# Kernel tuning notes

Measured on AMD Instinct MI355X. Metric: run time of the kernel, lower is better.

Reference implementation:

```python
import jax, jax.numpy as jnp
import numpy as np

B, S, I, H, O = 64, 512, 256, 1024, 256


def setup_inputs() -> dict:
    key = jax.random.key(0)
    ks = jax.random.split(key, 12)
    s_in = 1.0 / np.sqrt(H)  # torch RNN init scale
    inp = {
        "x": jax.random.normal(ks[0], (B, S, I), dtype=jnp.float32),
        "W_ih_0": jax.random.uniform(ks[1], (H, I), jnp.float32, -s_in, s_in),
        "W_hh_0": jax.random.uniform(ks[2], (H, H), jnp.float32, -s_in, s_in),
        "b_ih_0": jax.random.uniform(ks[3], (H,), jnp.float32, -s_in, s_in),
        "b_hh_0": jax.random.uniform(ks[4], (H,), jnp.float32, -s_in, s_in),
        "W_ih_1": jax.random.uniform(ks[5], (H, H), jnp.float32, -s_in, s_in),
        "W_hh_1": jax.random.uniform(ks[6], (H, H), jnp.float32, -s_in, s_in),
        "b_ih_1": jax.random.uniform(ks[7], (H,), jnp.float32, -s_in, s_in),
        "b_hh_1": jax.random.uniform(ks[8], (H,), jnp.float32, -s_in, s_in),
        "fc_w": jax.random.uniform(ks[9], (O, H), jnp.float32, -s_in, s_in),
        "fc_b": jax.random.uniform(ks[10], (O,), jnp.float32, -s_in, s_in),
    }
    return inp


def _rnn_layer(inp, W_ih, W_hh, b_ih, b_hh):
    # Pre-compute input projection for all timesteps (one big GEMM),
    # then scan the sequential recurrence: h_t = tanh(Wx_t + U h_{t-1} + b)
    pre = jnp.einsum('bsi,hi->bsh', inp, W_ih) + (b_ih + b_hh)  # [B,S,H]
    h0 = jnp.zeros((inp.shape[0], W_hh.shape[0]), dtype=inp.dtype)

    def step(h, p_t):
        h = jnp.tanh(p_t + h @ W_hh.T)
        return h, h

    _, hs = jax.lax.scan(step, h0, jnp.swapaxes(pre, 0, 1))  # [S,B,H]
    return jnp.swapaxes(hs, 0, 1)  # [B,S,H]


def reference(x, W_ih_0, W_hh_0, b_ih_0, b_hh_0,
              W_ih_1, W_hh_1, b_ih_1, b_hh_1, fc_w, fc_b):
    h = _rnn_layer(x, W_ih_0, W_hh_0, b_ih_0, b_hh_0)
    h = _rnn_layer(h, W_ih_1, W_hh_1, b_ih_1, b_hh_1)
    return h @ fc_w.T + fc_b  # [B,S,O]
```

## Files before the change

### kernel.cpp

```cpp
#include <hip/hip_runtime.h>
#include <hip/hip_bf16.h>


typedef __attribute__((ext_vector_type(4))) float f32x4;
typedef __attribute__((ext_vector_type(8))) short bf16x8;
typedef __attribute__((ext_vector_type(4))) int   i32x4;
typedef __attribute__((ext_vector_type(4))) short s16x4;

#define B_  64
#define S_  512
#define I_  256
#define H_  1024
#define O_  256
#define M_  (B_ * S_)
#define SH_ (S_ * H_)

static __device__ __forceinline__ unsigned short f2bf(float f) {
  union { float f; unsigned u; } v; v.f = f;
  unsigned r = v.u + 0x7fffu + ((v.u >> 16) & 1u);
  return (unsigned short)(r >> 16);
}
static __device__ __forceinline__ float bf2f(unsigned short b) {
  union { unsigned u; float f; } v; v.u = ((unsigned)b) << 16;
  return v.f;
}
static __device__ __forceinline__ float tanh_fast(float x) {
  float e = __expf(2.f * x);
  return 1.f - 2.f / (e + 1.f);
}
static __device__ __forceinline__ bf16x8 as_bf16x8(i32x4 v) {
  union { i32x4 i; bf16x8 b; } u; u.i = v; return u.b;
}

__global__ void cvt_bf16(const float* __restrict__ src,
                         unsigned short* __restrict__ dst, int n4) {
  int i = blockIdx.x * blockDim.x + threadIdx.x;
  if (i < n4) {
    f32x4 v = ((const f32x4*)src)[i];
    s16x4 o;
    o[0] = (short)f2bf(v[0]); o[1] = (short)f2bf(v[1]);
    o[2] = (short)f2bf(v[2]); o[3] = (short)f2bf(v[3]);
    ((s16x4*)dst)[i] = o;
  }
}

template <bool BF16OUT>
__global__ __launch_bounds__(256)
void gemm_bf16(const unsigned short* __restrict__ A,
               const unsigned short* __restrict__ W,
               const float* __restrict__ b1, const float* __restrict__ b2,
               void* __restrict__ Cv, int Mx, int Nx, int Kx) {
  __shared__ __align__(16) unsigned short As[128 * 40];
  __shared__ __align__(16) unsigned short Bs[128 * 40];
  const int tid  = threadIdx.x;
  const int m0   = blockIdx.y * 128;
  const int n0   = blockIdx.x * 128;
  const int w    = tid >> 6, lane = tid & 63;
  const int quad = lane >> 4, l15 = lane & 15;
  const int wm = (w & 1) * 64, wn = (w >> 1) * 64;

  f32x4 acc[4][4] = {};

  for (int k0 = 0; k0 < Kx; k0 += 32) {
#pragma unroll
    for (int i = 0; i < 2; ++i) {
      int c = tid + i * 256;
      int row = c >> 2, kc = c & 3;
      *(i32x4*)&As[row * 40 + kc * 8] =
          *(const i32x4*)&A[(size_t)(m0 + row) * Kx + k0 + kc * 8];
      *(i32x4*)&Bs[row * 40 + kc * 8] =
          *(const i32x4*)&W[(size_t)(n0 + row) * Kx + k0 + kc * 8];
    }
    __syncthreads();
    bf16x8 af[4], bg[4];
#pragma unroll
    for (int im = 0; im < 4; ++im)
      af[im] = *(const bf16x8*)&As[(wm + im * 16 + l15) * 40 + quad * 8];
#pragma unroll
    for (int in = 0; in < 4; ++in)
      bg[in] = *(const bf16x8*)&Bs[(wn + in * 16 + l15) * 40 + quad * 8];
#pragma unroll
    for (int im = 0; im < 4; ++im)
#pragma unroll
      for (int in = 0; in < 4; ++in)
        acc[im][in] = __builtin_amdgcn_mfma_f32_16x16x32_bf16(
            af[im], bg[in], acc[im][in], 0, 0, 0);
    __syncthreads();
  }

#pragma unroll
  for (int in = 0; in < 4; ++in) {
    int n = n0 + wn + in * 16 + l15;
    float bv = b1 ? b1[n] : 0.f;
    if (b2) bv += b2[n];
#pragma unroll
    for (int im = 0; im < 4; ++im) {
      int mb = m0 + wm + im * 16 + quad * 4;
#pragma unroll
      for (int r = 0; r < 4; ++r) {
        float val = acc[im][in][r] + bv;
        size_t o = (size_t)(mb + r) * Nx + n;
        if (BF16OUT) ((unsigned short*)Cv)[o] = f2bf(val);
        else         ((float*)Cv)[o] = val;
      }
    }
  }
}

__global__ __launch_bounds__(256, 1)
void rnn_fused(const unsigned short* __restrict__ Whh0,
               const unsigned short* __restrict__ Wih1,
               const unsigned short* __restrict__ Whh1,
               const unsigned short* __restrict__ pre0,
               const float* __restrict__ b_ih_1,
               const float* __restrict__ b_hh_1,
               unsigned short* __restrict__ h0seq,
               unsigned short* __restrict__ h1seq,
               unsigned int* __restrict__ flags)
{
  const int bx   = blockIdx.x;
  const int tid  = threadIdx.x;
  const int w    = tid >> 6;
  const int lane = tid & 63;
  const int quad = lane >> 4, l15 = lane & 15;

  __shared__ __align__(16) float q[4][4][16][20];

  if (bx < 64) {
    const int g  = bx >> 4;
    const int n0 = (bx & 15) * 64;
    unsigned int* const f0 = flags + g * S_;

    i32x4 Wf[4][8];
    {
      const unsigned short* wp = Whh0 + (size_t)(n0 + l15) * H_ + w * 256 + quad * 8;
#pragma unroll
      for (int i = 0; i < 4; ++i)
#pragma unroll
        for (int kk = 0; kk < 8; ++kk)
          Wf[i][kk] = *(const i32x4*)(wp + (size_t)i * 16 * H_ + kk * 32);
    }
#pragma unroll
    for (int i = 0; i < 4; ++i)
#pragma unroll
      for (int kk = 0; kk < 8; ++kk)
        asm volatile("" : "+v"(Wf[i][kk]));

    for (int t = 0; t < S_; ++t) {
      float pv[4];
      {
        const unsigned short* pp = pre0 + (size_t)(g * 16 + quad * 4) * SH_ +
                                   (size_t)t * H_ + n0 + w * 16 + l15;
#pragma unroll
        for (int r = 0; r < 4; ++r) pv[r] = bf2f(pp[(size_t)r * SH_]);
      }

      f32x4 acc[4] = {};
      if (t > 0) {
        if (tid == 0) {
          while (__hip_atomic_load(&f0[t - 1], __ATOMIC_RELAXED,
                                   __HIP_MEMORY_SCOPE_AGENT) < 16u) {}
          __builtin_amdgcn_fence(__ATOMIC_ACQUIRE, "agent");
        }
        __syncthreads();
        const unsigned short* hp = h0seq + (size_t)(g * 16 + l15) * SH_ +
                                   (size_t)(t - 1) * H_ + w * 256 + quad * 8;
        bf16x8 Af[8];
#pragma unroll
        for (int kk = 0; kk < 8; ++kk) Af[kk] = *(const bf16x8*)(hp + kk * 32);
#pragma unroll
        for (int kk = 0; kk < 8; ++kk)
#pragma unroll
          for (int i = 0; i < 4; ++i)
            acc[i] = __builtin_amdgcn_mfma_f32_16x16x32_bf16(
                Af[kk], as_bf16x8(Wf[i][kk]), acc[i], 0, 0, 0);
      }

#pragma unroll
      for (int i = 0; i < 4; ++i) *(f32x4*)&q[w][i][l15][quad * 4] = acc[i];
      __syncthreads();
      f32x4 s = {};
#pragma unroll
      for (int wp2 = 0; wp2 < 4; ++wp2) {
        f32x4 v = *(const f32x4*)&q[wp2][w][l15][quad * 4];
#pragma unroll
        for (int r = 0; r < 4; ++r) s[r] += v[r];
      }

#pragma unroll
      for (int r = 0; r < 4; ++r) {
        unsigned short hb = f2bf(tanh_fast(pv[r] + s[r]));
        size_t o = (size_t)(g * 16 + quad * 4 + r) * SH_ + (size_t)t * H_ +
                   n0 + w * 16 + l15;
        __hip_atomic_store(&h0seq[o], hb, __ATOMIC_RELAXED,
                           __HIP_MEMORY_SCOPE_AGENT);
      }
      __syncthreads();
      if (tid == 0)
        __hip_atomic_fetch_add(&f0[t], 1u, __ATOMIC_RELAXED,
                               __HIP_MEMORY_SCOPE_AGENT);
    }
  } else {
    const int id = bx - 64;
    const int g  = id >> 5;
    const int n0 = (id & 31) * 32;
    unsigned int* const f0 = flags + g * S_;
    unsigned int* const f1 = flags + 4 * S_ + g * S_;

    i32x4 Wi[2][8], Wr[2][8];
    {
      const unsigned short* wpi = Wih1 + (size_t)(n0 + l15) * H_ + w * 256 + quad * 8;
      const unsigned short* wpr = Whh1 + (size_t)(n0 + l15) * H_ + w * 256 + quad * 8;
#pragma unroll
      for (int i = 0; i < 2; ++i)
#pragma unroll
        for (int kk = 0; kk < 8; ++kk) {
          Wi[i][kk] = *(const i32x4*)(wpi + (size_t)i * 16 * H_ + kk * 32);
          Wr[i][kk] = *(const i32x4*)(wpr + (size_t)i * 16 * H_ + kk * 32);
        }
    }
#pragma unroll
    for (int i = 0; i < 2; ++i)
#pragma unroll
      for (int kk = 0; kk < 8; ++kk) {
        asm volatile("" : "+v"(Wi[i][kk]));
        asm volatile("" : "+v"(Wr[i][kk]));
      }

    float bias = 0.f;
    if (w < 2) {
      int n = n0 + w * 16 + l15;
      bias = b_ih_1[n] + b_hh_1[n];
    }

    for (int t = 0; t < S_; ++t) {
      f32x4 acc[2] = {};

      if (tid == 0) {
        while (__hip_atomic_load(&f0[t], __ATOMIC_RELAXED,
                                 __HIP_MEMORY_SCOPE_AGENT) < 16u) {}
        __builtin_amdgcn_fence(__ATOMIC_ACQUIRE, "agent");
      }
      __syncthreads();
      {
        const unsigned short* hp = h0seq + (size_t)(g * 16 + l15) * SH_ +
                                   (size_t)t * H_ + w * 256 + quad * 8;
        bf16x8 Af[8];
#pragma unroll
        for (int kk = 0; kk < 8; ++kk) Af[kk] = *(const bf16x8*)(hp + kk * 32);
#pragma unroll
        for (int kk = 0; kk < 8; ++kk)
#pragma unroll
          for (int i = 0; i < 2; ++i)
            acc[i] = __builtin_amdgcn_mfma_f32_16x16x32_bf16(
                Af[kk], as_bf16x8(Wi[i][kk]), acc[i], 0, 0, 0);
      }

      if (t > 0) {
        if (tid == 0) {
          while (__hip_atomic_load(&f1[t - 1], __ATOMIC_RELAXED,
                                   __HIP_MEMORY_SCOPE_AGENT) < 32u) {}
          __builtin_amdgcn_fence(__ATOMIC_ACQUIRE, "agent");
        }
        __syncthreads();
        const unsigned short* hp = h1seq + (size_t)(g * 16 + l15) * SH_ +
                                   (size_t)(t - 1) * H_ + w * 256 + quad * 8;
        bf16x8 Af[8];
#pragma unroll
        for (int kk = 0; kk < 8; ++kk) Af[kk] = *(const bf16x8*)(hp + kk * 32);
#pragma unroll
        for (int kk = 0; kk < 8; ++kk)
#pragma unroll
          for (int i = 0; i < 2; ++i)
            acc[i] = __builtin_amdgcn_mfma_f32_16x16x32_bf16(
                Af[kk], as_bf16x8(Wr[i][kk]), acc[i], 0, 0, 0);
      }

#pragma unroll
      for (int i = 0; i < 2; ++i) *(f32x4*)&q[w][i][l15][quad * 4] = acc[i];
      __syncthreads();
      if (w < 2) {
        f32x4 s = {};
#pragma unroll
        for (int wp2 = 0; wp2 < 4; ++wp2) {
          f32x4 v = *(const f32x4*)&q[wp2][w][l15][quad * 4];
#pragma unroll
          for (int r = 0; r < 4; ++r) s[r] += v[r];
        }
#pragma unroll
        for (int r = 0; r < 4; ++r) {
          unsigned short hb = f2bf(tanh_fast(bias + s[r]));
          size_t o = (size_t)(g * 16 + quad * 4 + r) * SH_ + (size_t)t * H_ +
                     n0 + w * 16 + l15;
          __hip_atomic_store(&h1seq[o], hb, __ATOMIC_RELAXED,
                             __HIP_MEMORY_SCOPE_AGENT);
        }
      }
      __syncthreads();
      if (tid == 0)
        __hip_atomic_fetch_add(&f1[t], 1u, __ATOMIC_RELAXED,
                               __HIP_MEMORY_SCOPE_AGENT);
    }
  }
}

extern "C" void kernel_launch(void* const* d_in, const int* in_sizes, int n_in,
                              void* d_out, int out_size, void* d_ws, size_t ws_size,
                              hipStream_t stream) {
  const float* x      = (const float*)d_in[0];
  const float* W_ih_0 = (const float*)d_in[1];
  const float* W_hh_0 = (const float*)d_in[2];
  const float* b_ih_0 = (const float*)d_in[3];
  const float* b_hh_0 = (const float*)d_in[4];
  const float* W_ih_1 = (const float*)d_in[5];
  const float* W_hh_1 = (const float*)d_in[6];
  const float* b_ih_1 = (const float*)d_in[7];
  const float* b_hh_1 = (const float*)d_in[8];
  const float* fc_w   = (const float*)d_in[9];
  const float* fc_b   = (const float*)d_in[10];
  float* out = (float*)d_out;

  char* ws = (char*)d_ws;
  size_t off = 0;
  auto alloc = [&](size_t bytes) { char* p = ws + off; off += (bytes + 255) & ~(size_t)255; return p; };
  unsigned short* xb    = (unsigned short*)alloc((size_t)M_ * I_ * 2);
  unsigned short* wih0b = (unsigned short*)alloc((size_t)H_ * I_ * 2);
  unsigned short* whh0b = (unsigned short*)alloc((size_t)H_ * H_ * 2);
  unsigned short* wih1b = (unsigned short*)alloc((size_t)H_ * H_ * 2);
  unsigned short* whh1b = (unsigned short*)alloc((size_t)H_ * H_ * 2);
  unsigned short* fcwb  = (unsigned short*)alloc((size_t)O_ * H_ * 2);
  unsigned int*   flags = (unsigned int*)alloc(2 * 4 * S_ * 4);
  unsigned short* pre0b = (unsigned short*)alloc((size_t)M_ * H_ * 2);
  unsigned short* h0seq = (unsigned short*)alloc((size_t)M_ * H_ * 2);
  unsigned short* h1seq = (unsigned short*)alloc((size_t)M_ * H_ * 2);

  hipMemsetAsync(flags, 0, 2 * 4 * S_ * 4, stream);

  auto cvt = [&](const float* s, unsigned short* d, int n) {
    int n4 = n / 4;
    cvt_bf16<<<(n4 + 255) / 256, 256, 0, stream>>>(s, d, n4);
  };
  cvt(x,      xb,    M_ * I_);
  cvt(W_ih_0, wih0b, H_ * I_);
  cvt(W_hh_0, whh0b, H_ * H_);
  cvt(W_ih_1, wih1b, H_ * H_);
  cvt(W_hh_1, whh1b, H_ * H_);
  cvt(fc_w,   fcwb,  O_ * H_);

  gemm_bf16<true><<<dim3(H_ / 128, M_ / 128), 256, 0, stream>>>(
      xb, wih0b, b_ih_0, b_hh_0, pre0b, M_, H_, I_);

  rnn_fused<<<192, 256, 0, stream>>>(whh0b, wih1b, whh1b, pre0b,
                                     b_ih_1, b_hh_1, h0seq, h1seq, flags);

  gemm_bf16<false><<<dim3(O_ / 128, M_ / 128), 256, 0, stream>>>(
      h1seq, fcwb, fc_b, nullptr, out, M_, O_, H_);
}
```

Baseline: 2.813 ms.

## Pin each RNN batch group to one XCD and use per-block step signals

Launches 256 blocks and keeps only even residues mod 8, so each batch group is meant to land on a single XCD. A startup handshake reads the hardware XCC id to confirm this placement. When placement is confirmed, hidden-state stores become plain stores instead of agent-scope atomics. Per-producer monotonic signal slots with min-polling and s_sleep replace the shared fetch-add counters. Layer-1 blocks now each cover 64 columns instead of 32, using all four waves. This adds a placement check with a timeout fallback. Plain stores rely on the XCD-local L2 being coherent for other blocks on the same XCD, and layer-1 register pressure is higher.

```diff
diff --git a/kernel.cpp b/kernel.cpp
--- a/kernel.cpp
+++ b/kernel.cpp
@@ -14,6 +14,8 @@
 #define O_  256
 #define M_  (B_ * S_)
 #define SH_ (S_ * H_)
+#define NACT 128
+#define POISON_TAG 0xFFu
 
 static __device__ __forceinline__ unsigned short f2bf(float f) {
   union { float f; unsigned u; } v; v.f = f;
@@ -30,6 +32,33 @@
 }
 static __device__ __forceinline__ bf16x8 as_bf16x8(i32x4 v) {
   union { i32x4 i; bf16x8 b; } u; u.i = v; return u.b;
+}
+
+
+static __device__ __forceinline__ void wait16(const unsigned* sig, int v) {
+  for (;;) {
+    unsigned mn = 0xffffffffu;
+#pragma unroll
+    for (int i = 0; i < 16; ++i) {
+      unsigned x = __hip_atomic_load(&sig[i], __ATOMIC_RELAXED,
+                                     __HIP_MEMORY_SCOPE_AGENT);
+      mn = x < mn ? x : mn;
+    }
+    if (mn >= (unsigned)v) break;
+    __builtin_amdgcn_s_sleep(2);
+  }
+  __builtin_amdgcn_fence(__ATOMIC_ACQUIRE, "agent");
+}
+
+static __device__ __forceinline__ void sig_store(unsigned* p, int v) {
+  __hip_atomic_store(p, (unsigned)v, __ATOMIC_RELAXED,
+                     __HIP_MEMORY_SCOPE_AGENT);
+}
+
+static __device__ __forceinline__ void h_store(unsigned short* p,
+                                               unsigned short v, bool local) {
+  if (local) *p = v;
+  else __hip_atomic_store(p, v, __ATOMIC_RELAXED, __HIP_MEMORY_SCOPE_AGENT);
 }
 
 __global__ void cvt_bf16(const float* __restrict__ src,
@@ -118,22 +147,71 @@
                unsigned short* __restrict__ h1seq,
                unsigned int* __restrict__ flags)
 {
-  const int bx   = blockIdx.x;
-  const int tid  = threadIdx.x;
+  const int bx  = blockIdx.x;
+  const int res = bx & 7;
+  if (res & 1) return;
+  const int g   = res >> 1;
+  const int r   = bx >> 3;
+  const int tid = threadIdx.x;
   const int w    = tid >> 6;
   const int lane = tid & 63;
   const int quad = lane >> 4, l15 = lane & 15;
-
+  const int n0   = (r & 15) * 64;
+
+  unsigned* xcdtab = flags;
+  unsigned* sigA = flags + 128 + (g * 3 + 0) * 16;
+  unsigned* sigB = flags + 128 + (g * 3 + 1) * 16;
+  unsigned* sigC = flags + 128 + (g * 3 + 2) * 16;
+
+  __shared__ int s_local;
   __shared__ __align__(16) float q[4][4][16][20];
 
-  if (bx < 64) {
-    const int g  = bx >> 4;
-    const int n0 = (bx & 15) * 64;
-    unsigned int* const f0 = flags + g * S_;
-
+  if (tid == 0) {
+    unsigned tag =
+        ((unsigned)__builtin_amdgcn_s_getreg((3 << 11) | 20) & 0xFu) + 1u;
+    __hip_atomic_store(&xcdtab[g * 32 + r], tag, __ATOMIC_RELEASE,
+                       __HIP_MEMORY_SCOPE_AGENT);
+    unsigned long long t0 = __builtin_amdgcn_s_memrealtime();
+    bool timeout = false;
+    for (;;) {
+      bool all = true;
+      for (int i = 0; i < NACT; ++i)
+        if (__hip_atomic_load(&xcdtab[i], __ATOMIC_RELAXED,
+                              __HIP_MEMORY_SCOPE_AGENT) == 0u) {
+          all = false; break;
+        }
+      if (all) break;
+      if (__builtin_amdgcn_s_memrealtime() - t0 > 5000000ull) {
+        timeout = true; break;
+      }
+      __builtin_amdgcn_s_sleep(8);
+    }
+    int verdict = 0;
+    if (timeout) {
+      __hip_atomic_store(&xcdtab[g * 32 + r], POISON_TAG, __ATOMIC_RELAXED,
+                         __HIP_MEMORY_SCOPE_AGENT);
+    } else {
+      __builtin_amdgcn_fence(__ATOMIC_ACQUIRE, "agent");
+      bool loc = true;
+      int  cnt = 0;
+      for (int i = 0; i < NACT; ++i) {
+        unsigned v = __hip_atomic_load(&xcdtab[i], __ATOMIC_RELAXED,
+                                       __HIP_MEMORY_SCOPE_AGENT);
+        if ((i >> 5) == g) loc &= (v == tag);
+        cnt += (v == tag) ? 1 : 0;
+      }
+      verdict = (loc && cnt == 32) ? 1 : 0;
+    }
+    s_local = verdict;
+  }
+  __syncthreads();
+  const bool local = (s_local != 0);
+
+  if (r < 16) {
     i32x4 Wf[4][8];
     {
-      const unsigned short* wp = Whh0 + (size_t)(n0 + l15) * H_ + w * 256 + quad * 8;
+      const unsigned short* wp =
+          Whh0 + (size_t)(n0 + l15) * H_ + w * 256 + quad * 8;
 #pragma unroll
       for (int i = 0; i < 4; ++i)
 #pragma unroll
@@ -152,16 +230,12 @@
         const unsigned short* pp = pre0 + (size_t)(g * 16 + quad * 4) * SH_ +
                                    (size_t)t * H_ + n0 + w * 16 + l15;
 #pragma unroll
-        for (int r = 0; r < 4; ++r) pv[r] = bf2f(pp[(size_t)r * SH_]);
+        for (int u = 0; u < 4; ++u) pv[u] = bf2f(pp[(size_t)u * SH_]);
       }
 
       f32x4 acc[4] = {};
       if (t > 0) {
-        if (tid == 0) {
-          while (__hip_atomic_load(&f0[t - 1], __ATOMIC_RELAXED,
-                                   __HIP_MEMORY_SCOPE_AGENT) < 16u) {}
-          __builtin_amdgcn_fence(__ATOMIC_ACQUIRE, "agent");
-        }
+        if (tid == 0) wait16(sigA, t);
         __syncthreads();
         const unsigned short* hp = h0seq + (size_t)(g * 16 + l15) * SH_ +
                                    (size_t)(t - 1) * H_ + w * 256 + quad * 8;
@@ -184,35 +258,32 @@
       for (int wp2 = 0; wp2 < 4; ++wp2) {
         f32x4 v = *(const f32x4*)&q[wp2][w][l15][quad * 4];
 #pragma unroll
-        for (int r = 0; r < 4; ++r) s[r] += v[r];
-      }
-
-#pragma unroll
-      for (int r = 0; r < 4; ++r) {
-        unsigned short hb = f2bf(tanh_fast(pv[r] + s[r]));
-        size_t o = (size_t)(g * 16 + quad * 4 + r) * SH_ + (size_t)t * H_ +
+        for (int u = 0; u < 4; ++u) s[u] += v[u];
+      }
+
+#pragma unroll
+      for (int u = 0; u < 4; ++u) {
+        unsigned short hb = f2bf(tanh_fast(pv[u] + s[u]));
+        size_t o = (size_t)(g * 16 + quad * 4 + u) * SH_ + (size_t)t * H_ +
                    n0 + w * 16 + l15;
-        __hip_atomic_store(&h0seq[o], hb, __ATOMIC_RELAXED,
-                           __HIP_MEMORY_SCOPE_AGENT);
+        h_store(&h0seq[o], hb, local);
       }
       __syncthreads();
-      if (tid == 0)
-        __hip_atomic_fetch_add(&f0[t], 1u, __ATOMIC_RELAXED,
-                               __HIP_MEMORY_SCOPE_AGENT);
+      if (tid == 0) {
+        sig_store(&sigA[r], t + 1);
+        sig_store(&sigB[r], t + 1);
+      }
     }
   } else {
-    const int id = bx - 64;
-    const int g  = id >> 5;
-    const int n0 = (id & 31) * 32;
-    unsigned int* const f0 = flags + g * S_;
-    unsigned int* const f1 = flags + 4 * S_ + g * S_;
-
-    i32x4 Wi[2][8], Wr[2][8];
+    const int p1 = r - 16;
+    i32x4 Wi[4][8], Wr[4][8];
     {
-      const unsigned short* wpi = Wih1 + (size_t)(n0 + l15) * H_ + w * 256 + quad * 8;
-      const unsigned short* wpr = Whh1 + (size_t)(n0 + l15) * H_ + w * 256 + quad * 8;
-#pragma unroll
-      for (int i = 0; i < 2; ++i)
+      const unsigned short* wpi =
+          Wih1 + (size_t)(n0 + l15) * H_ + w * 256 + quad * 8;
+      const unsigned short* wpr =
+          Whh1 + (size_t)(n0 + l15) * H_ + w * 256 + quad * 8;
+#pragma unroll
+      for (int i = 0; i < 4; ++i)
 #pragma unroll
         for (int kk = 0; kk < 8; ++kk) {
           Wi[i][kk] = *(const i32x4*)(wpi + (size_t)i * 16 * H_ + kk * 32);
@@ -220,27 +291,23 @@
         }
     }
 #pragma unroll
-    for (int i = 0; i < 2; ++i)
+    for (int i = 0; i < 4; ++i)
 #pragma unroll
       for (int kk = 0; kk < 8; ++kk) {
         asm volatile("" : "+v"(Wi[i][kk]));
         asm volatile("" : "+v"(Wr[i][kk]));
       }
 
-    float bias = 0.f;
-    if (w < 2) {
+    float bias;
+    {
       int n = n0 + w * 16 + l15;
       bias = b_ih_1[n] + b_hh_1[n];
     }
 
     for (int t = 0; t < S_; ++t) {
-      f32x4 acc[2] = {};
-
-      if (tid == 0) {
-        while (__hip_atomic_load(&f0[t], __ATOMIC_RELAXED,
-                                 __HIP_MEMORY_SCOPE_AGENT) < 16u) {}
-        __builtin_amdgcn_fence(__ATOMIC_ACQUIRE, "agent");
-      }
+      f32x4 acc[4] = {};
+
+      if (tid == 0) wait16(sigB, t + 1);
       __syncthreads();
       {
         const unsigned short* hp = h0seq + (size_t)(g * 16 + l15) * SH_ +
@@ -251,17 +318,13 @@
 #pragma unroll
         for (int kk = 0; kk < 8; ++kk)
 #pragma unroll
-          for (int i = 0; i < 2; ++i)
+          for (int i = 0; i < 4; ++i)
             acc[i] = __builtin_amdgcn_mfma_f32_16x16x32_bf16(
                 Af[kk], as_bf16x8(Wi[i][kk]), acc[i], 0, 0, 0);
       }
 
       if (t > 0) {
-        if (tid == 0) {
-          while (__hip_atomic_load(&f1[t - 1], __ATOMIC_RELAXED,
-                                   __HIP_MEMORY_SCOPE_AGENT) < 32u) {}
-          __builtin_amdgcn_fence(__ATOMIC_ACQUIRE, "agent");
-        }
+        if (tid == 0) wait16(sigC, t);
         __syncthreads();
         const unsigned short* hp = h1seq + (size_t)(g * 16 + l15) * SH_ +
                                    (size_t)(t - 1) * H_ + w * 256 + quad * 8;
@@ -271,35 +334,30 @@
 #pragma unroll
         for (int kk = 0; kk < 8; ++kk)
 #pragma unroll
-          for (int i = 0; i < 2; ++i)
+          for (int i = 0; i < 4; ++i)
             acc[i] = __builtin_amdgcn_mfma_f32_16x16x32_bf16(
                 Af[kk], as_bf16x8(Wr[i][kk]), acc[i], 0, 0, 0);
       }
 
 #pragma unroll
-      for (int i = 0; i < 2; ++i) *(f32x4*)&q[w][i][l15][quad * 4] = acc[i];
+      for (int i = 0; i < 4; ++i) *(f32x4*)&q[w][i][l15][quad * 4] = acc[i];
       __syncthreads();
-      if (w < 2) {
-        f32x4 s = {};
-#pragma unroll
-        for (int wp2 = 0; wp2 < 4; ++wp2) {
-          f32x4 v = *(const f32x4*)&q[wp2][w][l15][quad * 4];
-#pragma unroll
-          for (int r = 0; r < 4; ++r) s[r] += v[r];
-        }
-#pragma unroll
-        for (int r = 0; r < 4; ++r) {
-          unsigned short hb = f2bf(tanh_fast(bias + s[r]));
-          size_t o = (size_t)(g * 16 + quad * 4 + r) * SH_ + (size_t)t * H_ +
-                     n0 + w * 16 + l15;
-          __hip_atomic_store(&h1seq[o], hb, __ATOMIC_RELAXED,
-                             __HIP_MEMORY_SCOPE_AGENT);
-        }
+      f32x4 s = {};
+#pragma unroll
+      for (int wp2 = 0; wp2 < 4; ++wp2) {
+        f32x4 v = *(const f32x4*)&q[wp2][w][l15][quad * 4];
+#pragma unroll
+        for (int u = 0; u < 4; ++u) s[u] += v[u];
+      }
+#pragma unroll
+      for (int u = 0; u < 4; ++u) {
+        unsigned short hb = f2bf(tanh_fast(bias + s[u]));
+        size_t o = (size_t)(g * 16 + quad * 4 + u) * SH_ + (size_t)t * H_ +
+                   n0 + w * 16 + l15;
+        h_store(&h1seq[o], hb, local);
       }
       __syncthreads();
-      if (tid == 0)
-        __hip_atomic_fetch_add(&f1[t], 1u, __ATOMIC_RELAXED,
-                               __HIP_MEMORY_SCOPE_AGENT);
+      if (tid == 0) sig_store(&sigC[p1], t + 1);
     }
   }
 }
@@ -329,12 +387,12 @@
   unsigned short* wih1b = (unsigned short*)alloc((size_t)H_ * H_ * 2);
   unsigned short* whh1b = (unsigned short*)alloc((size_t)H_ * H_ * 2);
   unsigned short* fcwb  = (unsigned short*)alloc((size_t)O_ * H_ * 2);
-  unsigned int*   flags = (unsigned int*)alloc(2 * 4 * S_ * 4);
+  unsigned int*   flags = (unsigned int*)alloc(320 * 4);
   unsigned short* pre0b = (unsigned short*)alloc((size_t)M_ * H_ * 2);
   unsigned short* h0seq = (unsigned short*)alloc((size_t)M_ * H_ * 2);
   unsigned short* h1seq = (unsigned short*)alloc((size_t)M_ * H_ * 2);
 
-  hipMemsetAsync(flags, 0, 2 * 4 * S_ * 4, stream);
+  hipMemsetAsync(flags, 0, 320 * 4, stream);
 
   auto cvt = [&](const float* s, unsigned short* d, int n) {
     int n4 = n / 4;
@@ -350,7 +408,7 @@
   gemm_bf16<true><<<dim3(H_ / 128, M_ / 128), 256, 0, stream>>>(
       xb, wih0b, b_ih_0, b_hh_0, pre0b, M_, H_, I_);
 
-  rnn_fused<<<192, 256, 0, stream>>>(whh0b, wih1b, whh1b, pre0b,
+  rnn_fused<<<256, 256, 0, stream>>>(whh0b, wih1b, whh1b, pre0b,
                                      b_ih_1, b_hh_1, h0seq, h1seq, flags);
 
   gemm_bf16<false><<<dim3(O_ / 128, M_ / 128), 256, 0, stream>>>(
```

New measurement: 4.914 ms. 74.7% more time.

## Stage recurrent weights in LDS and load hidden state with cache-bypass loads

Applied to the files above, without the earlier changes.

Moves the per-block recurrent weight slices from pinned VGPRs into a 128KB LDS buffer read on every MFMA. Hidden-state reads now go through inline asm global loads with sc0 sc1 bits, so they are served from a coherent cache level rather than a possibly stale L2. It also adds an explicit vmcnt drain and release ordering on the flag increment so the producer's stores are visible before consumers are signalled. This frees many registers and fixes a cross-block visibility hazard, but adds LDS traffic and waits in the serial per-step critical path.

```diff
diff --git a/kernel.cpp b/kernel.cpp
--- a/kernel.cpp
+++ b/kernel.cpp
@@ -30,6 +30,28 @@
 }
 static __device__ __forceinline__ bf16x8 as_bf16x8(i32x4 v) {
   union { i32x4 i; bf16x8 b; } u; u.i = v; return u.b;
+}
+
+static __device__ __forceinline__ void load8_llc(const unsigned short* p,
+                                                 i32x4* o) {
+  asm volatile(
+      "global_load_dwordx4 %0, %8, off sc0 sc1\n\t"
+      "global_load_dwordx4 %1, %8, off offset:64 sc0 sc1\n\t"
+      "global_load_dwordx4 %2, %8, off offset:128 sc0 sc1\n\t"
+      "global_load_dwordx4 %3, %8, off offset:192 sc0 sc1\n\t"
+      "global_load_dwordx4 %4, %8, off offset:256 sc0 sc1\n\t"
+      "global_load_dwordx4 %5, %8, off offset:320 sc0 sc1\n\t"
+      "global_load_dwordx4 %6, %8, off offset:384 sc0 sc1\n\t"
+      "global_load_dwordx4 %7, %8, off offset:448 sc0 sc1\n\t"
+      "s_waitcnt vmcnt(0)"
+      : "=&v"(o[0]), "=&v"(o[1]), "=&v"(o[2]), "=&v"(o[3]),
+        "=&v"(o[4]), "=&v"(o[5]), "=&v"(o[6]), "=&v"(o[7])
+      : "v"(p)
+      : "memory");
+}
+
+static __device__ __forceinline__ void drain_stores() {
+  asm volatile("s_waitcnt vmcnt(0)" ::: "memory");
 }
 
 __global__ void cvt_bf16(const float* __restrict__ src,
@@ -124,6 +146,7 @@
   const int lane = tid & 63;
   const int quad = lane >> 4, l15 = lane & 15;
 
+  __shared__ __align__(16) unsigned short Wlds[65536];
   __shared__ __align__(16) float q[4][4][16][20];
 
   if (bx < 64) {
@@ -131,20 +154,16 @@
     const int n0 = (bx & 15) * 64;
     unsigned int* const f0 = flags + g * S_;
 
-    i32x4 Wf[4][8];
     {
       const unsigned short* wp = Whh0 + (size_t)(n0 + l15) * H_ + w * 256 + quad * 8;
 #pragma unroll
       for (int i = 0; i < 4; ++i)
 #pragma unroll
         for (int kk = 0; kk < 8; ++kk)
-          Wf[i][kk] = *(const i32x4*)(wp + (size_t)i * 16 * H_ + kk * 32);
-    }
-#pragma unroll
-    for (int i = 0; i < 4; ++i)
-#pragma unroll
-      for (int kk = 0; kk < 8; ++kk)
-        asm volatile("" : "+v"(Wf[i][kk]));
+          *(i32x4*)&Wlds[((w * 32 + i * 8 + kk) * 64 + lane) * 8] =
+              *(const i32x4*)(wp + (size_t)i * 16 * H_ + kk * 32);
+    }
+    __syncthreads();
 
     for (int t = 0; t < S_; ++t) {
       float pv[4];
@@ -163,17 +182,17 @@
           __builtin_amdgcn_fence(__ATOMIC_ACQUIRE, "agent");
         }
         __syncthreads();
-        const unsigned short* hp = h0seq + (size_t)(g * 16 + l15) * SH_ +
-                                   (size_t)(t - 1) * H_ + w * 256 + quad * 8;
-        bf16x8 Af[8];
-#pragma unroll
-        for (int kk = 0; kk < 8; ++kk) Af[kk] = *(const bf16x8*)(hp + kk * 32);
+        i32x4 Af[8];
+        load8_llc(h0seq + (size_t)(g * 16 + l15) * SH_ +
+                      (size_t)(t - 1) * H_ + w * 256 + quad * 8, Af);
 #pragma unroll
         for (int kk = 0; kk < 8; ++kk)
 #pragma unroll
           for (int i = 0; i < 4; ++i)
             acc[i] = __builtin_amdgcn_mfma_f32_16x16x32_bf16(
-                Af[kk], as_bf16x8(Wf[i][kk]), acc[i], 0, 0, 0);
+                as_bf16x8(Af[kk]),
+                *(const bf16x8*)&Wlds[((w * 32 + i * 8 + kk) * 64 + lane) * 8],
+                acc[i], 0, 0, 0);
       }
 
 #pragma unroll
@@ -195,9 +214,10 @@
         __hip_atomic_store(&h0seq[o], hb, __ATOMIC_RELAXED,
                            __HIP_MEMORY_SCOPE_AGENT);
       }
+      drain_stores();
       __syncthreads();
       if (tid == 0)
-        __hip_atomic_fetch_add(&f0[t], 1u, __ATOMIC_RELAXED,
+        __hip_atomic_fetch_add(&f0[t], 1u, __ATOMIC_RELEASE,
                                __HIP_MEMORY_SCOPE_AGENT);
     }
   } else {
@@ -207,7 +227,6 @@
     unsigned int* const f0 = flags + g * S_;
     unsigned int* const f1 = flags + 4 * S_ + g * S_;
 
-    i32x4 Wi[2][8], Wr[2][8];
     {
       const unsigned short* wpi = Wih1 + (size_t)(n0 + l15) * H_ + w * 256 + quad * 8;
       const unsigned short* wpr = Whh1 + (size_t)(n0 + l15) * H_ + w * 256 + quad * 8;
@@ -215,17 +234,13 @@
       for (int i = 0; i < 2; ++i)
 #pragma unroll
         for (int kk = 0; kk < 8; ++kk) {
-          Wi[i][kk] = *(const i32x4*)(wpi + (size_t)i * 16 * H_ + kk * 32);
-          Wr[i][kk] = *(const i32x4*)(wpr + (size_t)i * 16 * H_ + kk * 32);
-        }
-    }
-#pragma unroll
-    for (int i = 0; i < 2; ++i)
-#pragma unroll
-      for (int kk = 0; kk < 8; ++kk) {
-        asm volatile("" : "+v"(Wi[i][kk]));
-        asm volatile("" : "+v"(Wr[i][kk]));
-      }
+          *(i32x4*)&Wlds[((w * 16 + i * 8 + kk) * 64 + lane) * 8] =
+              *(const i32x4*)(wpi + (size_t)i * 16 * H_ + kk * 32);
+          *(i32x4*)&Wlds[32768 + ((w * 16 + i * 8 + kk) * 64 + lane) * 8] =
+              *(const i32x4*)(wpr + (size_t)i * 16 * H_ + kk * 32);
+        }
+    }
+    __syncthreads();
 
     float bias = 0.f;
     if (w < 2) {
@@ -243,17 +258,17 @@
       }
       __syncthreads();
       {
-        const unsigned short* hp = h0seq + (size_t)(g * 16 + l15) * SH_ +
-                                   (size_t)t * H_ + w * 256 + quad * 8;
-        bf16x8 Af[8];
-#pragma unroll
-        for (int kk = 0; kk < 8; ++kk) Af[kk] = *(const bf16x8*)(hp + kk * 32);
+        i32x4 Af[8];
+        load8_llc(h0seq + (size_t)(g * 16 + l15) * SH_ +
+                      (size_t)t * H_ + w * 256 + quad * 8, Af);
 #pragma unroll
         for (int kk = 0; kk < 8; ++kk)
 #pragma unroll
           for (int i = 0; i < 2; ++i)
             acc[i] = __builtin_amdgcn_mfma_f32_16x16x32_bf16(
-                Af[kk], as_bf16x8(Wi[i][kk]), acc[i], 0, 0, 0);
+                as_bf16x8(Af[kk]),
+                *(const bf16x8*)&Wlds[((w * 16 + i * 8 + kk) * 64 + lane) * 8],
+                acc[i], 0, 0, 0);
       }
 
       if (t > 0) {
@@ -263,17 +278,18 @@
           __builtin_amdgcn_fence(__ATOMIC_ACQUIRE, "agent");
         }
         __syncthreads();
-        const unsigned short* hp = h1seq + (size_t)(g * 16 + l15) * SH_ +
-                                   (size_t)(t - 1) * H_ + w * 256 + quad * 8;
-        bf16x8 Af[8];
-#pragma unroll
-        for (int kk = 0; kk < 8; ++kk) Af[kk] = *(const bf16x8*)(hp + kk * 32);
+        i32x4 Af[8];
+        load8_llc(h1seq + (size_t)(g * 16 + l15) * SH_ +
+                      (size_t)(t - 1) * H_ + w * 256 + quad * 8, Af);
 #pragma unroll
         for (int kk = 0; kk < 8; ++kk)
 #pragma unroll
           for (int i = 0; i < 2; ++i)
             acc[i] = __builtin_amdgcn_mfma_f32_16x16x32_bf16(
-                Af[kk], as_bf16x8(Wr[i][kk]), acc[i], 0, 0, 0);
+                as_bf16x8(Af[kk]),
+                *(const bf16x8*)&Wlds[32768 +
+                    ((w * 16 + i * 8 + kk) * 64 + lane) * 8],
+                acc[i], 0, 0, 0);
       }
 
 #pragma unroll
@@ -296,9 +312,10 @@
                              __HIP_MEMORY_SCOPE_AGENT);
         }
       }
+      drain_stores();
       __syncthreads();
       if (tid == 0)
-        __hip_atomic_fetch_add(&f1[t], 1u, __ATOMIC_RELAXED,
+        __hip_atomic_fetch_add(&f1[t], 1u, __ATOMIC_RELEASE,
                                __HIP_MEMORY_SCOPE_AGENT);
     }
   }
```

After: 4.236 ms. +50.6%, slower.
